# Performance work log

Hardware: AMD Instinct MI355X
Metric: run time of the kernel (lower is better)

## Reference

```python
import math
import jax, jax.numpy as jnp
import numpy as np

N_HEADS = 16  # matches init_kwargs n_heads

def setup_inputs() -> dict:
    key = jax.random.key(0)
    ks = jax.random.split(key, 6)
    B, T, D = 1, 2048, 1024
    x = jax.random.normal(ks[0], (B, T, D), dtype=jnp.float32)
    # binary causal mask, broadcast over batch: [B, T, T]
    mask = jnp.broadcast_to(jnp.tril(jnp.ones((T, T), dtype=jnp.float32)), (B, T, T))
    shift = jax.random.uniform(ks[1], (B, T, T), dtype=jnp.float32)
    W = jax.random.normal(ks[2], (D, 3 * D), dtype=jnp.float32) * (1.0 / math.sqrt(D))
    b = jnp.zeros((3 * D,), dtype=jnp.float32)
    Wo = jax.random.normal(ks[3], (D, D), dtype=jnp.float32) * (1.0 / math.sqrt(D))
    bo = jnp.zeros((D,), dtype=jnp.float32)
    return {"x": x, "mask": mask, "shift": shift, "W": W, "b": b, "Wo": Wo, "bo": bo}

def reference(x, mask, shift, W, b, Wo, bo):
    B, T, D = x.shape
    H = N_HEADS
    dh = D // H
    qkv = x @ W + b  # [B,T,3D]
    # torch: chunk(H) -> stack -> chunk(3): head h uses block [h*3*dh : (h+1)*3*dh],
    # split as (q, k, v) of size dh each => reshape last dim to (H, 3, dh)
    qkv = qkv.reshape(B, T, H, 3, dh)
    q = jnp.moveaxis(qkv[..., 0, :], 2, 0)  # [H,B,T,dh]
    k = jnp.moveaxis(qkv[..., 1, :], 2, 0)
    v = jnp.moveaxis(qkv[..., 2, :], 2, 0)
    logits = jnp.einsum('hbqd,hbkd->hbqk', q, k) / math.sqrt(dh)  # [H,B,T,T]
    logits = logits * mask - 1e6 * (1.0 - mask)  # mask [B,T,T] broadcasts over H
    # per-head ALiBi-like scale: exp(-log(2) * h / 2)
    scale = jnp.exp(-math.log(2.0) * jnp.arange(H, dtype=jnp.float32) / 2.0)
    logits = logits - scale.reshape(H, 1, 1, 1) * shift
    att = jax.nn.softmax(logits, axis=-1)
    o = jnp.einsum('hbqk,hbkd->hbqd', att, v)  # [H,B,T,dh]
    o = jnp.moveaxis(o, 0, 2).reshape(B, T, D)  # concat heads on last dim
    o = o @ Wo + bo
    k_out = jnp.moveaxis(k, 0, 2).reshape(B, T, D)
    v_out = jnp.moveaxis(v, 0, 2).reshape(B, T, D)
    return (o, k_out, v_out)
```

## Files before the change

kernel.cpp:

```cpp
#include <hip/hip_runtime.h>
#include <hip/hip_bf16.h>

typedef __attribute__((ext_vector_type(8))) short bfrag8;
typedef __attribute__((ext_vector_type(4))) float f32x4;
typedef __attribute__((ext_vector_type(8))) unsigned short ushort8;
typedef __attribute__((ext_vector_type(4))) unsigned short ushort4v;
typedef __attribute__((ext_vector_type(4))) unsigned int uint4v;

__device__ __forceinline__ float bf2f(unsigned short u) {
  unsigned int v = ((unsigned int)u) << 16;
  return __builtin_bit_cast(float, v);
}
__device__ __forceinline__ unsigned short f2bf(float f) {
  unsigned int u = __builtin_bit_cast(unsigned int, f);
  u += 0x7fffu + ((u >> 16) & 1u);
  return (unsigned short)(u >> 16);
}
__device__ __forceinline__ unsigned int cvtpk_bf16(float a, float b) {
  unsigned int r;
  asm("v_cvt_pk_bf16_f32 %0, %1, %2" : "=v"(r) : "v"(a), "v"(b));
  return r;
}

#define GLDS(gp, lp) __builtin_amdgcn_global_load_lds( \
    (__attribute__((address_space(1))) void*)(gp), \
    (__attribute__((address_space(3))) void*)(lp), 16, 0, 0)

#define WAIT_LGKM0() __builtin_amdgcn_s_waitcnt(0xc07f)

__device__ __forceinline__ bool inputs_are_f32(const unsigned int* mw) {
  return mw[0] == 0x3F800000u;
}

__global__ __launch_bounds__(256) void prep_kernel(
    const void* __restrict__ x, const void* __restrict__ b,
    const void* __restrict__ bo, const void* __restrict__ W,
    const void* __restrict__ Wo,
    unsigned short* __restrict__ xc, unsigned short* __restrict__ bc,
    unsigned short* __restrict__ boc, unsigned short* __restrict__ Wt,
    unsigned short* __restrict__ Wot,
    const unsigned int* __restrict__ mw) {
  const bool isf32 = inputs_are_f32(mw);
  const int bid = blockIdx.x, tid = threadIdx.x;
  __shared__ unsigned short tile[64][68];

  if (bid < 2052) {
    const void* src; unsigned short* dst; int base, n4;
    if (bid < 2048)      { src = x;  dst = xc;  base = bid;        n4 = 2048 * 1024 / 4; }
    else if (bid < 2051) { src = b;  dst = bc;  base = bid - 2048; n4 = 3072 / 4; }
    else                 { src = bo; dst = boc; base = 0;          n4 = 1024 / 4; }
    int i = base * 256 + tid;
    if (i >= n4) return;
    ushort4v o;
    if (isf32) {
      const float* s = (const float*)src;
      o[0] = f2bf(s[i * 4 + 0]); o[1] = f2bf(s[i * 4 + 1]);
      o[2] = f2bf(s[i * 4 + 2]); o[3] = f2bf(s[i * 4 + 3]);
    } else {
      o = *(const ushort4v*)((const unsigned short*)src + (size_t)i * 4);
    }
    *(ushort4v*)(dst + (size_t)i * 4) = o;
    return;
  }

  const void* src; unsigned short* dst; int R, C, bx, by;
  if (bid < 2820) { src = W;  dst = Wt;  R = 1024; C = 3072;
                    int e = bid - 2052; bx = e % 48; by = e / 48; }
  else            { src = Wo; dst = Wot; R = 1024; C = 1024;
                    int e = bid - 2820; bx = e % 16; by = e / 16; }
  const int r0 = by << 6, c0 = bx << 6;
  #pragma unroll
  for (int i = 0; i < 4; ++i) {
    int e = i * 256 + tid;
    int r = e >> 4, c4 = (e & 15) << 2;
    size_t idx = (size_t)(r0 + r) * C + c0 + c4;
    if (isf32) {
      f32x4 v = *(const f32x4*)((const float*)src + idx);
      tile[r][c4 + 0] = f2bf(v[0]); tile[r][c4 + 1] = f2bf(v[1]);
      tile[r][c4 + 2] = f2bf(v[2]); tile[r][c4 + 3] = f2bf(v[3]);
    } else {
      ushort4v v = *(const ushort4v*)((const unsigned short*)src + idx);
      tile[r][c4 + 0] = v[0]; tile[r][c4 + 1] = v[1];
      tile[r][c4 + 2] = v[2]; tile[r][c4 + 3] = v[3];
    }
  }
  __syncthreads();
  #pragma unroll
  for (int i = 0; i < 4; ++i) {
    int e = i * 256 + tid;
    int c = e >> 4, r4 = (e & 15) << 2;
    ushort4v o;
    o[0] = tile[r4 + 0][c]; o[1] = tile[r4 + 1][c];
    o[2] = tile[r4 + 2][c]; o[3] = tile[r4 + 3][c];
    *(ushort4v*)(dst + (size_t)(c0 + c) * R + r0 + r4) = o;
  }
}

template <int BM, int BN, int BK, int EPI>
__global__ __launch_bounds__(256) void gemm_bt(
    const unsigned short* __restrict__ A,
    const unsigned short* __restrict__ Bt,
    const unsigned short* __restrict__ bias,
    unsigned short* __restrict__ Cbf,
    float* __restrict__ kout,
    float* __restrict__ vout,
    float* __restrict__ Cf,
    int M, int N, int K) {
  constexpr int MI = BM / 32;
  constexpr int NT = BN / 32;
  constexpr int CW = BK / 8;
  __shared__ __align__(16) unsigned short As[BM * BK];
  __shared__ __align__(16) unsigned short Bs[BN * BK];
  const int tid = threadIdx.x;
  const int wave = tid >> 6, lane = tid & 63;
  const int q8 = lane >> 4, l15 = lane & 15;
  const int m0 = blockIdx.y * BM, n0 = blockIdx.x * BN;
  const int wm = (wave >> 1) * (BM / 2), wn = (wave & 1) * (BN / 2);
  const int swz = l15 & 7;

  f32x4 acc[MI][NT];
  #pragma unroll
  for (int i = 0; i < MI; ++i)
    #pragma unroll
    for (int t = 0; t < NT; ++t) acc[i][t] = (f32x4){0.f, 0.f, 0.f, 0.f};

  const int cidb = wave * 64 + lane;
  for (int k0 = 0; k0 < K; k0 += BK) {
    __syncthreads();
    #pragma unroll
    for (int j = 0; j < (BM * BK) / 2048; ++j) {
      int cid = j * 256 + cidb;
      int row = cid / CW, p = cid % CW;
      GLDS(A + (size_t)(m0 + row) * K + k0 + ((p ^ (row & 7)) << 3),
           As + (size_t)(j * 256 + wave * 64) * 8);
    }
    #pragma unroll
    for (int j = 0; j < (BN * BK) / 2048; ++j) {
      int cid = j * 256 + cidb;
      int row = cid / CW, p = cid % CW;
      GLDS(Bt + (size_t)(n0 + row) * K + k0 + ((p ^ (row & 7)) << 3),
           Bs + (size_t)(j * 256 + wave * 64) * 8);
    }
    __builtin_amdgcn_s_waitcnt(0);
    __syncthreads();
    #pragma unroll
    for (int kk = 0; kk < BK / 32; ++kk) {
      const int kc = kk * 4 + q8;
      bfrag8 af[MI], bfr[NT];
      #pragma unroll
      for (int i = 0; i < MI; ++i)
        af[i] = *(const bfrag8*)(As + (size_t)(wm + i * 16 + l15) * BK + ((kc ^ swz) << 3));
      #pragma unroll
      for (int t = 0; t < NT; ++t)
        bfr[t] = *(const bfrag8*)(Bs + (size_t)(wn + t * 16 + l15) * BK + ((kc ^ swz) << 3));
      #pragma unroll
      for (int i = 0; i < MI; ++i)
        #pragma unroll
        for (int t = 0; t < NT; ++t)
          acc[i][t] = __builtin_amdgcn_mfma_f32_16x16x32_bf16(af[i], bfr[t], acc[i][t], 0, 0, 0);
    }
  }

  #pragma unroll
  for (int t = 0; t < NT; ++t) {
    const int col = n0 + wn + t * 16 + l15;
    const float bv = bf2f(bias[col]);
    #pragma unroll
    for (int i = 0; i < MI; ++i) {
      #pragma unroll
      for (int r = 0; r < 4; ++r) {
        const int row = m0 + wm + i * 16 + q8 * 4 + r;
        const float fv = acc[i][t][r] + bv;
        if (EPI) {
          Cbf[(size_t)row * N + col] = f2bf(fv);
          int h = col / 192, rr = col - h * 192;
          if (rr >= 128)      vout[(size_t)row * 1024 + h * 64 + (rr - 128)] = fv;
          else if (rr >= 64)  kout[(size_t)row * 1024 + h * 64 + (rr - 64)] = fv;
        } else {
          Cf[(size_t)row * N + col] = fv;
        }
      }
    }
  }
}

__global__ __launch_bounds__(256) void attn_kernel(
    const unsigned short* __restrict__ qkv,
    const void* __restrict__ shift,
    unsigned short* __restrict__ Pon,
    float* __restrict__ Lst,
    const unsigned int* __restrict__ mw) {
  const bool isf32 = inputs_are_f32(mw);
  __shared__ __align__(16) unsigned short Qs[64 * 64];
  __shared__ __align__(16) unsigned short Ks[64 * 64];
  __shared__ __align__(16) unsigned short VTs[64 * 64];

  const int tid = threadIdx.x;
  const int wave = tid >> 6, lane = tid & 63;
  const int q8 = lane >> 4, l15 = lane & 15;
  int rem = blockIdx.x;
  int qb = 31;
  for (;;) { int seg = ((qb + 6) / 6) << 4; if (rem < seg) break; rem -= seg; --qb; }
  const int p = rem >> 4, h = rem & 15;
  const int q0 = qb << 6;
  const int count = qb + 1;
  const int kbeg = p * 6;
  const int kend = (kbeg + 6 < count) ? (kbeg + 6) : count;
  const float LOG2E = 1.4426950408889634f;
  const float c1 = 0.125f * LOG2E;
  const float scale2 = __builtin_amdgcn_exp2f(-0.5f * (float)h) * LOG2E;
  const float MFIX = 16.0f;
  const float NEG = -1e30f;
  const int moff0 = 0, moff1 = 32, moff2 = 4, moff3 = 36;
  const int base_l = ((l15 >> 2) << 3) + (l15 & 3);
  const int kread = l15 & 7;

  #pragma unroll
  for (int j = 0; j < 2; ++j) {
    int cid = j * 256 + wave * 64 + lane;
    int row = cid >> 3, ci = cid & 7;
    ushort8 qv = *(const ushort8*)(qkv + (size_t)(q0 + row) * 3072 + h * 192 + ci * 8);
    *(ushort8*)(Qs + row * 64 + ((ci ^ (row & 7)) << 3)) = qv;
  }

  const int cidA = wave * 64 + lane;
  const int rowA = cidA >> 3, ciA = cidA & 7;
  const int cidB = 256 + cidA;
  const int rowB = cidB >> 3, ciB = cidB & 7;
  const int kswzA = (rowA & 3) | ((rowA & 8) >> 1);
  const int kswzB = (rowB & 3) | ((rowB & 8) >> 1);

  float lrow = 0.f;
  f32x4 oacc[4];
  #pragma unroll
  for (int t = 0; t < 4; ++t) oacc[t] = (f32x4){0.f, 0.f, 0.f, 0.f};
  const int qg = q0 + wave * 16 + l15;

  ushort8 kpfA, kpfB, vpf0, vpf1;
  float shf[4][4];

  {
    const int k0 = kbeg << 6;
    kpfA = *(const ushort8*)(qkv + (size_t)(k0 + rowA) * 3072 + h * 192 + 64 + ciA * 8);
    kpfB = *(const ushort8*)(qkv + (size_t)(k0 + rowB) * 3072 + h * 192 + 64 + ciB * 8);
    const unsigned short* vsrc = qkv + (size_t)(k0 + lane) * 3072 + h * 192 + 128 + wave * 16;
    vpf0 = *(const ushort8*)(vsrc);
    vpf1 = *(const ushort8*)(vsrc + 8);
    if (isf32) {
      const float* sp = (const float*)shift + (size_t)qg * 2048 + k0 + q8 * 8;
      f32x4 t0 = *(const f32x4*)(sp + moff0);
      f32x4 t1 = *(const f32x4*)(sp + moff1);
      f32x4 t2 = *(const f32x4*)(sp + moff2);
      f32x4 t3 = *(const f32x4*)(sp + moff3);
      #pragma unroll
      for (int r = 0; r < 4; ++r) {
        shf[0][r] = scale2 * t0[r] + MFIX; shf[1][r] = scale2 * t1[r] + MFIX;
        shf[2][r] = scale2 * t2[r] + MFIX; shf[3][r] = scale2 * t3[r] + MFIX;
      }
    } else {
      const unsigned short* sp = (const unsigned short*)shift + (size_t)qg * 2048 + k0 + q8 * 8;
      ushort4v t0 = *(const ushort4v*)(sp + moff0);
      ushort4v t1 = *(const ushort4v*)(sp + moff1);
      ushort4v t2 = *(const ushort4v*)(sp + moff2);
      ushort4v t3 = *(const ushort4v*)(sp + moff3);
      #pragma unroll
      for (int r = 0; r < 4; ++r) {
        shf[0][r] = scale2 * bf2f(t0[r]) + MFIX; shf[1][r] = scale2 * bf2f(t1[r]) + MFIX;
        shf[2][r] = scale2 * bf2f(t2[r]) + MFIX; shf[3][r] = scale2 * bf2f(t3[r]) + MFIX;
      }
    }
  }

  for (int kt = kbeg; kt < kend; ++kt) {
    const int k0 = kt << 6;
    WAIT_LGKM0();
    __builtin_amdgcn_s_barrier();
    *(ushort8*)(Ks + rowA * 64 + ((ciA ^ kswzA) << 3)) = kpfA;
    *(ushort8*)(Ks + rowB * 64 + ((ciB ^ kswzB) << 3)) = kpfB;
    #pragma unroll
    for (int j = 0; j < 8; ++j) {
      int d = wave * 16 + j;
      VTs[d * 64 + (((lane >> 3) ^ (d & 7)) << 3) + (lane & 7)] = vpf0[j];
      int d2 = d + 8;
      VTs[d2 * 64 + (((lane >> 3) ^ (d2 & 7)) << 3) + (lane & 7)] = vpf1[j];
    }
    WAIT_LGKM0();
    __builtin_amdgcn_s_barrier();

    if (kt + 1 < kend) {
      const int k0n = k0 + 64;
      kpfA = *(const ushort8*)(qkv + (size_t)(k0n + rowA) * 3072 + h * 192 + 64 + ciA * 8);
      kpfB = *(const ushort8*)(qkv + (size_t)(k0n + rowB) * 3072 + h * 192 + 64 + ciB * 8);
      const unsigned short* vsrc = qkv + (size_t)(k0n + lane) * 3072 + h * 192 + 128 + wave * 16;
      vpf0 = *(const ushort8*)(vsrc);
      vpf1 = *(const ushort8*)(vsrc + 8);
    }

    f32x4 st[4];
    #pragma unroll
    for (int mt = 0; mt < 4; ++mt) st[mt] = (f32x4){0.f, 0.f, 0.f, 0.f};
    __builtin_amdgcn_s_setprio(1);
    #pragma unroll
    for (int kk = 0; kk < 2; ++kk) {
      int kc = kk * 4 + q8;
      int qrow = wave * 16 + l15;
      bfrag8 bq = *(const bfrag8*)(Qs + qrow * 64 + ((kc ^ (qrow & 7)) << 3));
      #pragma unroll
      for (int mt = 0; mt < 4; ++mt) {
        const int mo = (mt == 0) ? moff0 : (mt == 1) ? moff1 : (mt == 2) ? moff2 : moff3;
        int krow = base_l + mo;
        bfrag8 ak = *(const bfrag8*)(Ks + krow * 64 + ((kc ^ kread) << 3));
        st[mt] = __builtin_amdgcn_mfma_f32_16x16x32_bf16(ak, bq, st[mt], 0, 0, 0);
      }
    }
    __builtin_amdgcn_s_setprio(0);

    const bool diag = (kt == qb);
    float sv[4][4];
    #pragma unroll
    for (int mt = 0; mt < 4; ++mt) {
      const int mo = (mt == 0) ? moff0 : (mt == 1) ? moff1 : (mt == 2) ? moff2 : moff3;
      #pragma unroll
      for (int r = 0; r < 4; ++r) {
        float s = st[mt][r] * c1 - shf[mt][r];
        if (diag) {
          int kg = k0 + (q8 << 3) + mo + r;
          if (kg > qg) s = NEG;
        }
        float pv = __builtin_amdgcn_exp2f(s);
        sv[mt][r] = pv;
        lrow += pv;
      }
    }

    if (kt + 1 < kend) {
      const int k0n = k0 + 64;
      if (isf32) {
        const float* sp = (const float*)shift + (size_t)qg * 2048 + k0n + q8 * 8;
        f32x4 t0 = *(const f32x4*)(sp + moff0);
        f32x4 t1 = *(const f32x4*)(sp + moff1);
        f32x4 t2 = *(const f32x4*)(sp + moff2);
        f32x4 t3 = *(const f32x4*)(sp + moff3);
        #pragma unroll
        for (int r = 0; r < 4; ++r) {
          shf[0][r] = scale2 * t0[r] + MFIX; shf[1][r] = scale2 * t1[r] + MFIX;
          shf[2][r] = scale2 * t2[r] + MFIX; shf[3][r] = scale2 * t3[r] + MFIX;
        }
      } else {
        const unsigned short* sp = (const unsigned short*)shift + (size_t)qg * 2048 + k0n + q8 * 8;
        ushort4v t0 = *(const ushort4v*)(sp + moff0);
        ushort4v t1 = *(const ushort4v*)(sp + moff1);
        ushort4v t2 = *(const ushort4v*)(sp + moff2);
        ushort4v t3 = *(const ushort4v*)(sp + moff3);
        #pragma unroll
        for (int r = 0; r < 4; ++r) {
          shf[0][r] = scale2 * bf2f(t0[r]) + MFIX; shf[1][r] = scale2 * bf2f(t1[r]) + MFIX;
          shf[2][r] = scale2 * bf2f(t2[r]) + MFIX; shf[3][r] = scale2 * bf2f(t3[r]) + MFIX;
        }
      }
    }

    const unsigned int w00 = cvtpk_bf16(sv[0][0], sv[0][1]);
    const unsigned int w01 = cvtpk_bf16(sv[0][2], sv[0][3]);
    const unsigned int w10 = cvtpk_bf16(sv[1][0], sv[1][1]);
    const unsigned int w11 = cvtpk_bf16(sv[1][2], sv[1][3]);
    const unsigned int w20 = cvtpk_bf16(sv[2][0], sv[2][1]);
    const unsigned int w21 = cvtpk_bf16(sv[2][2], sv[2][3]);
    const unsigned int w30 = cvtpk_bf16(sv[3][0], sv[3][1]);
    const unsigned int w31 = cvtpk_bf16(sv[3][2], sv[3][3]);
    uint4v u0; u0[0] = w00; u0[1] = w01; u0[2] = w20; u0[3] = w21;
    uint4v u1; u1[0] = w10; u1[1] = w11; u1[2] = w30; u1[3] = w31;
    const bfrag8 ap0 = __builtin_bit_cast(bfrag8, u0);
    const bfrag8 ap1 = __builtin_bit_cast(bfrag8, u1);

    __builtin_amdgcn_s_setprio(1);
    #pragma unroll
    for (int kk = 0; kk < 2; ++kk) {
      int kc = kk * 4 + q8;
      const bfrag8 ap = kk ? ap1 : ap0;
      #pragma unroll
      for (int t = 0; t < 4; ++t) {
        int drow = t * 16 + l15;
        bfrag8 bv = *(const bfrag8*)(VTs + drow * 64 + ((kc ^ (drow & 7)) << 3));
        oacc[t] = __builtin_amdgcn_mfma_f32_16x16x32_bf16(ap, bv, oacc[t], 0, 0, 0);
      }
    }
    __builtin_amdgcn_s_setprio(0);
  }

  lrow += __shfl_xor(lrow, 16, 64);
  lrow += __shfl_xor(lrow, 32, 64);
  float linv[4];
  #pragma unroll
  for (int r = 0; r < 4; ++r) {
    float lr = __shfl(lrow, (lane & 48) | (q8 * 4 + r), 64);
    linv[r] = lr > 0.f ? 1.f / lr : 0.f;
  }
  const size_t slot = (size_t)(h * 32 + qb) * 6 + p;
  const size_t pbase = slot * 4096;
  #pragma unroll
  for (int t = 0; t < 4; ++t)
    #pragma unroll
    for (int r = 0; r < 4; ++r) {
      int rowl = wave * 16 + q8 * 4 + r;
      int coll = t * 16 + l15;
      Pon[pbase + rowl * 64 + coll] = f2bf(oacc[t][r] * linv[r]);
    }
  if (q8 == 0) {
    const size_t sbase = slot * 64 + wave * 16 + l15;
    Lst[sbase] = lrow;
  }
}

__global__ __launch_bounds__(256) void attn_merge(
    const unsigned short* __restrict__ Pon,
    const float* __restrict__ Lst,
    unsigned short* __restrict__ oheads) {
  const int bid = blockIdx.x;
  const int h = bid >> 5, qb = bid & 31;
  const int np = (qb + 6) / 6;
  const int t = threadIdx.x;
  const int q = t >> 2, dp = (t & 3) << 4;
  const size_t slot0 = (size_t)(h * 32 + qb) * 6;
  float w[6], wsum = 0.f;
  #pragma unroll
  for (int p = 0; p < 6; ++p) {
    w[p] = (p < np) ? Lst[(slot0 + p) * 64 + q] : 0.f;
    wsum += w[p];
  }
  const float inv = 1.f / wsum;
  float acc0[8], acc1[8];
  #pragma unroll
  for (int j = 0; j < 8; ++j) { acc0[j] = 0.f; acc1[j] = 0.f; }
  #pragma unroll
  for (int p = 0; p < 6; ++p) {
    if (p < np) {
      const unsigned short* pp = Pon + (slot0 + p) * 4096 + q * 64 + dp;
      ushort8 a0 = *(const ushort8*)pp;
      ushort8 a1 = *(const ushort8*)(pp + 8);
      #pragma unroll
      for (int j = 0; j < 8; ++j) {
        acc0[j] += w[p] * bf2f(a0[j]);
        acc1[j] += w[p] * bf2f(a1[j]);
      }
    }
  }
  unsigned short* dst = oheads + (size_t)(qb * 64 + q) * 1024 + h * 64 + dp;
  ushort8 o0, o1;
  #pragma unroll
  for (int j = 0; j < 8; ++j) {
    o0[j] = f2bf(acc0[j] * inv);
    o1[j] = f2bf(acc1[j] * inv);
  }
  *(ushort8*)dst = o0;
  *(ushort8*)(dst + 8) = o1;
}

extern "C" void kernel_launch(void* const* d_in, const int* in_sizes, int n_in,
                              void* d_out, int out_size, void* d_ws, size_t ws_size,
                              hipStream_t stream) {
  const void* x     = d_in[0];
  const unsigned int* maskw = (const unsigned int*)d_in[1];
  const void* shift = d_in[2];
  const void* W     = d_in[3];
  const void* b     = d_in[4];
  const void* Wo    = d_in[5];
  const void* bo    = d_in[6];

  float* out   = (float*)d_out;
  float* o_out = out;
  float* k_out = out + (size_t)2048 * 1024;
  float* v_out = out + (size_t)2 * 2048 * 1024;

  unsigned short* ws     = (unsigned short*)d_ws;
  unsigned short* qkv    = ws;
  unsigned short* Wot    = qkv + (size_t)2048 * 3072;
  unsigned short* oheads = Wot + (size_t)1024 * 1024;
  unsigned short* bc     = oheads + (size_t)2048 * 1024;
  unsigned short* boc    = bc + 3072;
  unsigned short* xc     = boc + 1024;
  unsigned short* Wt     = xc + (size_t)2048 * 1024;
  unsigned short* Pon    = xc;
  float*          Lst    = (float*)(Pon + (size_t)16 * 32 * 6 * 4096);

  prep_kernel<<<3076, 256, 0, stream>>>(x, b, bo, W, Wo,
                                        xc, bc, boc, Wt, Wot, maskw);

  gemm_bt<64, 128, 64, 1><<<dim3(24, 32), 256, 0, stream>>>(
      xc, Wt, bc, qkv, k_out, v_out, nullptr, 2048, 3072, 1024);

  attn_kernel<<<1632, 256, 0, stream>>>(qkv, shift, Pon, Lst, maskw);

  attn_merge<<<512, 256, 0, stream>>>(Pon, Lst, oheads);

  gemm_bt<64, 64, 64, 0><<<dim3(16, 32), 256, 0, stream>>>(
      oheads, Wot, boc, nullptr, nullptr, nullptr, o_out, 2048, 1024, 1024);
}
```

Measured before the change: 182.4 us.

## Double-buffer GEMM shared-memory tiles and widen prep conversion to 8 elements

The GEMM kernel now keeps two LDS buffers and issues the global-to-LDS loads for the next K tile before computing on the current one. It waits only on the older loads through a vmcnt-limited waitcnt, so memory latency can overlap with MFMA work. The prep kernel converts x and the biases 8 elements per thread with vector loads and stores, which halves the number of elementwise blocks. The cost is double the LDS per block, which may lower occupancy, and the hand-written waitcnt encoding has to count outstanding loads correctly.

```diff
diff --git a/kernel.cpp b/kernel.cpp
--- a/kernel.cpp
+++ b/kernel.cpp
@@ -27,6 +27,7 @@
     (__attribute__((address_space(3))) void*)(lp), 16, 0, 0)
 
 #define WAIT_LGKM0() __builtin_amdgcn_s_waitcnt(0xc07f)
+#define WAIT_VM(N) __builtin_amdgcn_s_waitcnt(0x0F70 | (N))
 
 __device__ __forceinline__ bool inputs_are_f32(const unsigned int* mw) {
   return mw[0] == 0x3F800000u;
@@ -44,30 +45,32 @@
   const int bid = blockIdx.x, tid = threadIdx.x;
   __shared__ unsigned short tile[64][68];
 
-  if (bid < 2052) {
-    const void* src; unsigned short* dst; int base, n4;
-    if (bid < 2048)      { src = x;  dst = xc;  base = bid;        n4 = 2048 * 1024 / 4; }
-    else if (bid < 2051) { src = b;  dst = bc;  base = bid - 2048; n4 = 3072 / 4; }
-    else                 { src = bo; dst = boc; base = 0;          n4 = 1024 / 4; }
+  if (bid < 1027) {
+    const void* src; unsigned short* dst; int base, n8;
+    if (bid < 1024)      { src = x;  dst = xc;  base = bid;        n8 = 2048 * 1024 / 8; }
+    else if (bid < 1026) { src = b;  dst = bc;  base = bid - 1024; n8 = 3072 / 8; }
+    else                 { src = bo; dst = boc; base = 0;          n8 = 1024 / 8; }
     int i = base * 256 + tid;
-    if (i >= n4) return;
-    ushort4v o;
+    if (i >= n8) return;
+    ushort8 o;
     if (isf32) {
-      const float* s = (const float*)src;
-      o[0] = f2bf(s[i * 4 + 0]); o[1] = f2bf(s[i * 4 + 1]);
-      o[2] = f2bf(s[i * 4 + 2]); o[3] = f2bf(s[i * 4 + 3]);
+      const float* s = (const float*)src + (size_t)i * 8;
+      f32x4 v0 = *(const f32x4*)(s);
+      f32x4 v1 = *(const f32x4*)(s + 4);
+      o[0] = f2bf(v0[0]); o[1] = f2bf(v0[1]); o[2] = f2bf(v0[2]); o[3] = f2bf(v0[3]);
+      o[4] = f2bf(v1[0]); o[5] = f2bf(v1[1]); o[6] = f2bf(v1[2]); o[7] = f2bf(v1[3]);
     } else {
-      o = *(const ushort4v*)((const unsigned short*)src + (size_t)i * 4);
-    }
-    *(ushort4v*)(dst + (size_t)i * 4) = o;
+      o = *(const ushort8*)((const unsigned short*)src + (size_t)i * 8);
+    }
+    *(ushort8*)(dst + (size_t)i * 8) = o;
     return;
   }
 
   const void* src; unsigned short* dst; int R, C, bx, by;
-  if (bid < 2820) { src = W;  dst = Wt;  R = 1024; C = 3072;
-                    int e = bid - 2052; bx = e % 48; by = e / 48; }
+  if (bid < 1795) { src = W;  dst = Wt;  R = 1024; C = 3072;
+                    int e = bid - 1027; bx = e % 48; by = e / 48; }
   else            { src = Wo; dst = Wot; R = 1024; C = 1024;
-                    int e = bid - 2820; bx = e % 16; by = e / 16; }
+                    int e = bid - 1795; bx = e % 16; by = e / 16; }
   const int r0 = by << 6, c0 = bx << 6;
   #pragma unroll
   for (int i = 0; i < 4; ++i) {
@@ -109,8 +112,11 @@
   constexpr int MI = BM / 32;
   constexpr int NT = BN / 32;
   constexpr int CW = BK / 8;
-  __shared__ __align__(16) unsigned short As[BM * BK];
-  __shared__ __align__(16) unsigned short Bs[BN * BK];
+  constexpr int AL = (BM * BK) / 2048;
+  constexpr int BL = (BN * BK) / 2048;
+  constexpr int LOADS = AL + BL;
+  __shared__ __align__(16) unsigned short As[2][BM * BK];
+  __shared__ __align__(16) unsigned short Bs[2][BN * BK];
   const int tid = threadIdx.x;
   const int wave = tid >> 6, lane = tid & 63;
   const int q8 = lane >> 4, l15 = lane & 15;
@@ -125,40 +131,52 @@
     for (int t = 0; t < NT; ++t) acc[i][t] = (f32x4){0.f, 0.f, 0.f, 0.f};
 
   const int cidb = wave * 64 + lane;
-  for (int k0 = 0; k0 < K; k0 += BK) {
-    __syncthreads();
-    #pragma unroll
-    for (int j = 0; j < (BM * BK) / 2048; ++j) {
+  auto stage = [&](int buf, int k0) {
+    #pragma unroll
+    for (int j = 0; j < AL; ++j) {
       int cid = j * 256 + cidb;
-      int row = cid / CW, p = cid % CW;
-      GLDS(A + (size_t)(m0 + row) * K + k0 + ((p ^ (row & 7)) << 3),
-           As + (size_t)(j * 256 + wave * 64) * 8);
-    }
-    #pragma unroll
-    for (int j = 0; j < (BN * BK) / 2048; ++j) {
+      int row = cid / CW, pp = cid % CW;
+      GLDS(A + (size_t)(m0 + row) * K + k0 + ((pp ^ (row & 7)) << 3),
+           &As[buf][(size_t)(j * 256 + wave * 64) * 8]);
+    }
+    #pragma unroll
+    for (int j = 0; j < BL; ++j) {
       int cid = j * 256 + cidb;
-      int row = cid / CW, p = cid % CW;
-      GLDS(Bt + (size_t)(n0 + row) * K + k0 + ((p ^ (row & 7)) << 3),
-           Bs + (size_t)(j * 256 + wave * 64) * 8);
-    }
-    __builtin_amdgcn_s_waitcnt(0);
-    __syncthreads();
+      int row = cid / CW, pp = cid % CW;
+      GLDS(Bt + (size_t)(n0 + row) * K + k0 + ((pp ^ (row & 7)) << 3),
+           &Bs[buf][(size_t)(j * 256 + wave * 64) * 8]);
+    }
+  };
+
+  const int nk = K / BK;
+  stage(0, 0);
+  for (int kt = 0; kt < nk; ++kt) {
+    const int cur = kt & 1;
+    if (kt + 1 < nk) {
+      stage(cur ^ 1, (kt + 1) * BK);
+      WAIT_VM(LOADS);
+    } else {
+      WAIT_VM(0);
+    }
+    __builtin_amdgcn_s_barrier();
     #pragma unroll
     for (int kk = 0; kk < BK / 32; ++kk) {
       const int kc = kk * 4 + q8;
       bfrag8 af[MI], bfr[NT];
       #pragma unroll
       for (int i = 0; i < MI; ++i)
-        af[i] = *(const bfrag8*)(As + (size_t)(wm + i * 16 + l15) * BK + ((kc ^ swz) << 3));
+        af[i] = *(const bfrag8*)(&As[cur][(size_t)(wm + i * 16 + l15) * BK + ((kc ^ swz) << 3)]);
       #pragma unroll
       for (int t = 0; t < NT; ++t)
-        bfr[t] = *(const bfrag8*)(Bs + (size_t)(wn + t * 16 + l15) * BK + ((kc ^ swz) << 3));
+        bfr[t] = *(const bfrag8*)(&Bs[cur][(size_t)(wn + t * 16 + l15) * BK + ((kc ^ swz) << 3)]);
       #pragma unroll
       for (int i = 0; i < MI; ++i)
         #pragma unroll
         for (int t = 0; t < NT; ++t)
           acc[i][t] = __builtin_amdgcn_mfma_f32_16x16x32_bf16(af[i], bfr[t], acc[i][t], 0, 0, 0);
     }
+    WAIT_LGKM0();
+    __builtin_amdgcn_s_barrier();
   }
 
   #pragma unroll
@@ -483,7 +501,7 @@
   unsigned short* Pon    = xc;
   float*          Lst    = (float*)(Pon + (size_t)16 * 32 * 6 * 4096);
 
-  prep_kernel<<<3076, 256, 0, stream>>>(x, b, bo, W, Wo,
+  prep_kernel<<<2051, 256, 0, stream>>>(x, b, bo, W, Wo,
                                         xc, bc, boc, Wt, Wot, maskw);
 
   gemm_bt<64, 128, 64, 1><<<dim3(24, 32), 256, 0, stream>>>(
```

After: 181.3 us (median of 2 runs). About the same (-0.6%).
